# Performance work log

Hardware: AMD Instinct MI355X
Metric: run time of the kernel (lower is better)

Reference implementation:

```python
import jax, jax.numpy as jnp
import numpy as np

B, F, V, D_EMB = 16384, 32, 50000, 16
D_IN = F * D_EMB            # 512, concat embedding dim
N_TASK, N_SPEC, N_SH = 2, 2, 2
E = N_TASK * N_SPEC + N_SH  # 6 experts per CGC level
H1, H2 = 512, 256           # expert_params dims
T1, T2 = 128, 64            # tower dims


def setup_inputs() -> dict:
    key = jax.random.key(0)
    ks = iter(jax.random.split(key, 32))
    def w(shape, s=0.05):
        return jax.random.normal(next(ks), shape, jnp.float32) * s
    return dict(
        x_ids=jax.random.randint(next(ks), (B, F), 0, V),
        emb=w((F, V, D_EMB)),
        e1_W1=w((E, D_IN, H1)), e1_b1=jnp.zeros((E, H1), jnp.float32),
        e1_W2=w((E, H1, H2)), e1_b2=jnp.zeros((E, H2), jnp.float32),
        g1_Ws=w((N_TASK, D_IN, N_SPEC + N_SH)), g1_bs=jnp.zeros((N_TASK, N_SPEC + N_SH), jnp.float32),
        g1_Wsh=w((D_IN, E)), g1_bsh=jnp.zeros((E,), jnp.float32),
        e2_W1=w((E, H2, H1)), e2_b1=jnp.zeros((E, H1), jnp.float32),
        e2_W2=w((E, H1, H2)), e2_b2=jnp.zeros((E, H2), jnp.float32),
        g2_Ws=w((N_TASK, H2, N_SPEC + N_SH)), g2_bs=jnp.zeros((N_TASK, N_SPEC + N_SH), jnp.float32),
        tw_W1=w((N_TASK, H2, T1)), tw_b1=jnp.zeros((N_TASK, T1), jnp.float32),
        tw_W2=w((N_TASK, T1, T2)), tw_b2=jnp.zeros((N_TASK, T2), jnp.float32),
    )


def _cgc(x_list, W1, b1, W2, b2, Wg, bg, Wg_sh=None, bg_sh=None):
    # Stack expert inputs: task-t specific experts read x_list[t], shared read x_list[-1].
    X = jnp.stack([x_list[0]] * N_SPEC + [x_list[1]] * N_SPEC + [x_list[-1]] * N_SH)  # [E,B,Din]
    # Grouped two-layer expert MLP (BatchNorm is identity at eval-mode init).
    h = jax.nn.relu(jnp.einsum('ebd,edh->ebh', X, W1) + b1[:, None, :])   # [E,B,H1]
    out = jax.nn.relu(jnp.einsum('ebh,eho->ebo', h, W2) + b2[:, None, :])  # [E,B,H2]
    outs = []
    for t in range(N_TASK):
        gate = jax.nn.softmax(x_list[t] @ Wg[t] + bg[t], axis=-1)          # [B, N_SPEC+N_SH]
        sel = jnp.concatenate([out[t * N_SPEC:(t + 1) * N_SPEC], out[-N_SH:]], axis=0)
        outs.append(jnp.einsum('bk,kbo->bo', gate, sel))
    if Wg_sh is not None:  # shared gate only for levels < n_level
        gate = jax.nn.softmax(x_list[-1] @ Wg_sh + bg_sh, axis=-1)          # [B,E]
        outs.append(jnp.einsum('bk,kbo->bo', gate, out))
    return outs


def reference(x_ids, emb, e1_W1, e1_b1, e1_W2, e1_b2, g1_Ws, g1_bs, g1_Wsh, g1_bsh,
              e2_W1, e2_b1, e2_W2, e2_b2, g2_Ws, g2_bs, tw_W1, tw_b1, tw_W2, tw_b2):
    # Embedding lookup per sparse feature, then flatten (squeeze_dim=True).
    embed_x = emb[jnp.arange(F)[None, :], x_ids].reshape(B, D_IN)  # [B, 512]
    xs = [embed_x] * (N_TASK + 1)
    xs = _cgc(xs, e1_W1, e1_b1, e1_W2, e1_b2, g1_Ws, g1_bs, g1_Wsh, g1_bsh)  # level 1 -> 3 outs
    xs = _cgc(xs, e2_W1, e2_b1, e2_W2, e2_b2, g2_Ws, g2_bs)                  # level 2 -> 2 outs
    ys = []
    for t in range(N_TASK):
        h = jax.nn.relu(xs[t] @ tw_W1[t] + tw_b1[t])
        h = jax.nn.relu(h @ tw_W2[t] + tw_b2[t])
        ys.append(jax.nn.sigmoid(h))  # PredictionLayer('classification')
    return jnp.concatenate(ys, axis=1)  # [B, N_TASK*T2]
```

## Files before the change

### kernel.cpp

```cpp
#include <hip/hip_runtime.h>

typedef unsigned short u16;
typedef __attribute__((ext_vector_type(4))) unsigned short u16x4;
typedef __attribute__((ext_vector_type(8))) unsigned short u16x8;
typedef __attribute__((ext_vector_type(8))) short s16x8;
typedef __attribute__((ext_vector_type(4))) float f32x4;

#define BATCH 16384
#define NFEAT 32
#define NVOCAB 50000

__device__ __forceinline__ u16 f2bf(float f) {
    union { float f; unsigned u; } v; v.f = f;
    unsigned u = v.u;
    return (u16)((u + 0x7fffu + ((u >> 16) & 1u)) >> 16);
}
__device__ __forceinline__ float bf2f(u16 h) {
    union { unsigned u; float f; } v; v.u = ((unsigned)h) << 16;
    return v.f;
}

__device__ __forceinline__ void load_lds16(const u16* g, u16* l) {
    __builtin_amdgcn_global_load_lds(
        (const __attribute__((address_space(1))) void*)g,
        (__attribute__((address_space(3))) void*)l, 16, 0, 0);
}

struct PrepDesc { const float* src; u16* dst; int K; int N; int nz; int zbase; };
struct PrepArgs { PrepDesc d[6]; };

__global__ void prep_weights(PrepArgs args) {
    int z = blockIdx.z;
    int di = 0;
    #pragma unroll
    for (int i = 0; i < 6; i++)
        if (z >= args.d[i].zbase && z < args.d[i].zbase + args.d[i].nz) di = i;
    PrepDesc d = args.d[di];
    int zz = z - d.zbase;
    int k0 = blockIdx.x * 32, n0 = blockIdx.y * 32;
    if (k0 >= d.K || n0 >= d.N) return;
    __shared__ float tile[32][33];
    const float* src = d.src + (long)zz * d.K * d.N;
    u16* dst = d.dst + (long)zz * d.K * d.N;
    int tx = threadIdx.x & 31, ty = threadIdx.x >> 5;
    for (int r = ty; r < 32; r += 8) {
        int k = k0 + r, n = n0 + tx;
        tile[r][tx] = (k < d.K && n < d.N) ? src[(long)k * d.N + n] : 0.f;
    }
    __syncthreads();
    for (int r = ty; r < 32; r += 8) {
        int n = n0 + r, k = k0 + tx;
        if (n < d.N && k < d.K) dst[(long)n * d.K + k] = f2bf(tile[tx][r]);
    }
}

__global__ void gather_embed(const int* __restrict__ ids,
                             const float* __restrict__ emb,
                             u16* __restrict__ out) {
    int idx = blockIdx.x * 256 + threadIdx.x;
    int d4 = idx & 3;
    int f  = (idx >> 2) & 31;
    int b  = idx >> 7;
    int id = ids[b * NFEAT + f];
    const float4* p = (const float4*)(emb + ((long)f * NVOCAB + id) * 16) + d4;
    float4 v = *p;
    u16x4 o;
    o.x = f2bf(v.x); o.y = f2bf(v.y); o.z = f2bf(v.z); o.w = f2bf(v.w);
    *(u16x4*)(out + (long)b * 512 + f * 16 + d4 * 4) = o;
}

struct GemmP {
    const u16* A; const u16* Bt; const float* bias; u16* C;
    int N, K, a_zshift, c_row_stride; long a_zstride, c_zstride;
};

__device__ __forceinline__ void gemm_impl(const GemmP p) {
    __shared__ u16 sA[128 * 64];
    __shared__ u16 sB[256 * 64];
    const int z = blockIdx.z;
    const u16* Ab = p.A + (long)(z >> p.a_zshift) * p.a_zstride;
    const u16* Bb = p.Bt + (long)z * p.N * p.K;
    const int m0 = blockIdx.x * 128;
    const int n0 = blockIdx.y * 256;
    const int tid = threadIdx.x;
    const int lane = tid & 63;
    const int w = tid >> 6;
    const int wm = (w & 1) * 64;
    const int wn = (w >> 1) * 128;
    const int l16 = lane & 15;
    const int q = lane >> 4;
    const int key = l16 & 7;
    const int K = p.K;

    const int tr = tid >> 3;
    const int lc = (tid & 7) ^ (tr & 7);
    const u16* gA0 = Ab + (long)(m0 + tr) * K + lc * 8;
    const u16* gB0 = Bb + (long)(n0 + tr) * K + lc * 8;
    u16* lA0 = &sA[(tid & ~63) * 8];
    u16* lB0 = &sB[(tid & ~63) * 8];

    f32x4 acc[4][8] = {};

    for (int k0 = 0; k0 < K; k0 += 64) {
        if (k0) __syncthreads();
        #pragma unroll
        for (int i = 0; i < 4; i++)
            load_lds16(gA0 + (long)(32 * i) * K + k0, lA0 + i * 256 * 8);
        #pragma unroll
        for (int i = 0; i < 8; i++)
            load_lds16(gB0 + (long)(32 * i) * K + k0, lB0 + i * 256 * 8);
        __syncthreads();
        #pragma unroll
        for (int kk = 0; kk < 2; kk++) {
            const int pc = ((kk << 2) | q) ^ key;
            s16x8 af[4], bf[8];
            #pragma unroll
            for (int mt = 0; mt < 4; mt++)
                af[mt] = *(const s16x8*)(&sA[(wm + mt * 16 + l16) * 64 + pc * 8]);
            #pragma unroll
            for (int nt = 0; nt < 8; nt++)
                bf[nt] = *(const s16x8*)(&sB[(wn + nt * 16 + l16) * 64 + pc * 8]);
            #pragma unroll
            for (int mt = 0; mt < 4; mt++)
                #pragma unroll
                for (int nt = 0; nt < 8; nt++)
                    acc[mt][nt] = __builtin_amdgcn_mfma_f32_16x16x32_bf16(
                        bf[nt], af[mt], acc[mt][nt], 0, 0, 0);
        }
    }

    const float* bb = p.bias + (long)z * p.N;
    u16* Cp = p.C + (long)z * p.c_zstride;
    #pragma unroll
    for (int mt = 0; mt < 4; mt++) {
        int grow = m0 + wm + mt * 16 + l16;
        u16* rowp = Cp + (long)grow * p.c_row_stride;
        #pragma unroll
        for (int nt = 0; nt < 8; nt++) {
            int gc = n0 + wn + nt * 16 + q * 4;
            float4 bv = *(const float4*)(bb + gc);
            f32x4 v = acc[mt][nt];
            v.x = fmaxf(v.x + bv.x, 0.f);
            v.y = fmaxf(v.y + bv.y, 0.f);
            v.z = fmaxf(v.z + bv.z, 0.f);
            v.w = fmaxf(v.w + bv.w, 0.f);
            u16x4 o;
            o.x = f2bf(v.x); o.y = f2bf(v.y); o.z = f2bf(v.z); o.w = f2bf(v.w);
            *(u16x4*)(rowp + gc) = o;
        }
    }
}

__global__ __launch_bounds__(256, 2) void gemm_l1a(GemmP p) { gemm_impl(p); }
__global__ __launch_bounds__(256, 2) void gemm_l1b(GemmP p) { gemm_impl(p); }
__global__ __launch_bounds__(256, 2) void gemm_l2a(GemmP p) { gemm_impl(p); }
__global__ __launch_bounds__(256, 2) void gemm_l2b(GemmP p) { gemm_impl(p); }

__global__ __launch_bounds__(256, 1)
void tower_fused(const u16* __restrict__ x2, const u16* __restrict__ W1t,
                 const float* __restrict__ b1, const u16* __restrict__ W2t,
                 const float* __restrict__ b2, float* __restrict__ out) {
    const int t = blockIdx.y, m0 = blockIdx.x * 64;
    __shared__ u16 sX[64 * 256];
    __shared__ u16 sW1[128 * 256];
    __shared__ u16 sH[64 * 136];
    __shared__ u16 sW2[64 * 128];
    __shared__ float sB1[128];
    __shared__ float sB2[64];
    const int tid = threadIdx.x, lane = tid & 63, w = tid >> 6;
    const int l16 = lane & 15, q = lane >> 4;

    #pragma unroll
    for (int i = 0; i < 8; i++) {
        int c = i * 256 + tid, row = c >> 5, kc = c & 31;
        int lcc = (kc & ~7) | ((kc & 7) ^ (row & 7));
        load_lds16(x2 + ((long)t * BATCH + m0 + row) * 256 + lcc * 8,
                   &sX[(i * 256 + (tid & ~63)) * 8]);
    }
    #pragma unroll
    for (int i = 0; i < 16; i++) {
        int c = i * 256 + tid, row = c >> 5, kc = c & 31;
        int lcc = (kc & ~7) | ((kc & 7) ^ (row & 7));
        load_lds16(W1t + ((long)t * 128 + row) * 256 + lcc * 8,
                   &sW1[(i * 256 + (tid & ~63)) * 8]);
    }
    #pragma unroll
    for (int i = 0; i < 4; i++) {
        int c = i * 256 + tid, row = c >> 4, kc = c & 15;
        int lcc = (kc & ~7) | ((kc & 7) ^ (row & 7));
        load_lds16(W2t + ((long)t * 64 + row) * 128 + lcc * 8,
                   &sW2[(i * 256 + (tid & ~63)) * 8]);
    }
    if (tid < 128) sB1[tid] = b1[t * 128 + tid];
    if (tid < 64)  sB2[tid] = b2[t * 64 + tid];
    __syncthreads();

    f32x4 acc1[4][2] = {};
    #pragma unroll
    for (int kk = 0; kk < 8; kk++) {
        int pcb = kk * 4 + q;
        s16x8 af[4], bf[2];
        #pragma unroll
        for (int mt = 0; mt < 4; mt++) {
            int row = mt * 16 + l16;
            int sc = (pcb & ~7) | ((pcb & 7) ^ (row & 7));
            af[mt] = *(const s16x8*)(&sX[row * 256 + sc * 8]);
        }
        #pragma unroll
        for (int nt = 0; nt < 2; nt++) {
            int row = w * 32 + nt * 16 + l16;
            int sc = (pcb & ~7) | ((pcb & 7) ^ (row & 7));
            bf[nt] = *(const s16x8*)(&sW1[row * 256 + sc * 8]);
        }
        #pragma unroll
        for (int mt = 0; mt < 4; mt++)
            #pragma unroll
            for (int nt = 0; nt < 2; nt++)
                acc1[mt][nt] = __builtin_amdgcn_mfma_f32_16x16x32_bf16(
                    bf[nt], af[mt], acc1[mt][nt], 0, 0, 0);
    }
    #pragma unroll
    for (int mt = 0; mt < 4; mt++) {
        int row = mt * 16 + l16;
        #pragma unroll
        for (int nt = 0; nt < 2; nt++) {
            int col = w * 32 + nt * 16 + q * 4;
            f32x4 v = acc1[mt][nt];
            u16x4 o;
            o.x = f2bf(fmaxf(v.x + sB1[col + 0], 0.f));
            o.y = f2bf(fmaxf(v.y + sB1[col + 1], 0.f));
            o.z = f2bf(fmaxf(v.z + sB1[col + 2], 0.f));
            o.w = f2bf(fmaxf(v.w + sB1[col + 3], 0.f));
            *(u16x4*)(&sH[row * 136 + col]) = o;
        }
    }
    __syncthreads();

    f32x4 acc2[4] = {};
    #pragma unroll
    for (int kk = 0; kk < 4; kk++) {
        s16x8 af[4], bf;
        #pragma unroll
        for (int mt = 0; mt < 4; mt++) {
            int row = mt * 16 + l16;
            af[mt] = *(const s16x8*)(&sH[row * 136 + kk * 32 + q * 8]);
        }
        {
            int row = w * 16 + l16;
            int pc = kk * 4 + q;
            int sc = (pc & ~7) | ((pc & 7) ^ (row & 7));
            bf = *(const s16x8*)(&sW2[row * 128 + sc * 8]);
        }
        #pragma unroll
        for (int mt = 0; mt < 4; mt++)
            acc2[mt] = __builtin_amdgcn_mfma_f32_16x16x32_bf16(
                bf, af[mt], acc2[mt], 0, 0, 0);
    }
    #pragma unroll
    for (int mt = 0; mt < 4; mt++) {
        int grow = m0 + mt * 16 + l16;
        int col = w * 16 + q * 4;
        float4 bv = *(const float4*)(sB2 + col);
        f32x4 v = acc2[mt];
        float4 r;
        r.x = 1.f / (1.f + __expf(-(v.x + bv.x)));
        r.y = 1.f / (1.f + __expf(-(v.y + bv.y)));
        r.z = 1.f / (1.f + __expf(-(v.z + bv.z)));
        r.w = 1.f / (1.f + __expf(-(v.w + bv.w)));
        *(float4*)(out + (long)grow * 128 + t * 64 + col) = r;
    }
}

__global__ __launch_bounds__(256)
void gate1(const u16* __restrict__ embed, const u16* __restrict__ out1,
           const float* __restrict__ g1Ws, const float* __restrict__ g1bs,
           const float* __restrict__ gWsh, const float* __restrict__ gbsh,
           u16* __restrict__ x1) {
    const int m0 = blockIdx.x * 64;
    __shared__ float sg[64][16];
    const int tid = threadIdx.x;
    const int row = tid >> 2, pp = tid & 3;

    float a[4] = {0, 0, 0, 0}, b[4] = {0, 0, 0, 0}, c[6] = {0, 0, 0, 0, 0, 0};
    const u16* er = embed + (long)(m0 + row) * 512 + pp * 128;
    const float* Wa = g1Ws;
    const float* Wb = g1Ws + 2048;
    for (int j = 0; j < 128; j += 8) {
        u16x8 xv8 = *(const u16x8*)(er + j);
        #pragma unroll
        for (int u = 0; u < 8; u++) {
            float xv = bf2f(xv8[u]);
            int k = pp * 128 + j + u;
            float4 wa = *(const float4*)(Wa + k * 4);
            float4 wb = *(const float4*)(Wb + k * 4);
            a[0] += xv * wa.x; a[1] += xv * wa.y; a[2] += xv * wa.z; a[3] += xv * wa.w;
            b[0] += xv * wb.x; b[1] += xv * wb.y; b[2] += xv * wb.z; b[3] += xv * wb.w;
            const float* wc = gWsh + k * 6;
            #pragma unroll
            for (int g = 0; g < 6; g++) c[g] += xv * wc[g];
        }
    }
    #pragma unroll
    for (int g = 0; g < 4; g++) {
        a[g] += __shfl_xor(a[g], 1); a[g] += __shfl_xor(a[g], 2);
        b[g] += __shfl_xor(b[g], 1); b[g] += __shfl_xor(b[g], 2);
    }
    #pragma unroll
    for (int g = 0; g < 6; g++) { c[g] += __shfl_xor(c[g], 1); c[g] += __shfl_xor(c[g], 2); }
    if (pp == 0) {
        float mx, s, e[6];
        mx = -1e30f;
        for (int g = 0; g < 4; g++) { a[g] += g1bs[g]; mx = fmaxf(mx, a[g]); }
        s = 0.f; for (int g = 0; g < 4; g++) { e[g] = __expf(a[g] - mx); s += e[g]; }
        for (int g = 0; g < 4; g++) sg[row][g] = e[g] / s;
        mx = -1e30f;
        for (int g = 0; g < 4; g++) { b[g] += g1bs[4 + g]; mx = fmaxf(mx, b[g]); }
        s = 0.f; for (int g = 0; g < 4; g++) { e[g] = __expf(b[g] - mx); s += e[g]; }
        for (int g = 0; g < 4; g++) sg[row][4 + g] = e[g] / s;
        mx = -1e30f;
        for (int g = 0; g < 6; g++) { c[g] += gbsh[g]; mx = fmaxf(mx, c[g]); }
        s = 0.f; for (int g = 0; g < 6; g++) { e[g] = __expf(c[g] - mx); s += e[g]; }
        for (int g = 0; g < 6; g++) sg[row][8 + g] = e[g] / s;
    }
    __syncthreads();

    for (int r = 0; r < 64; r++) {
        long rb = m0 + r;
        float o[6];
        #pragma unroll
        for (int k = 0; k < 6; k++)
            o[k] = bf2f(out1[((long)k * BATCH + rb) * 256 + tid]);
        const float* g = sg[r];
        float v0 = g[0] * o[0] + g[1] * o[1] + g[2] * o[4] + g[3] * o[5];
        float v1 = g[4] * o[2] + g[5] * o[3] + g[6] * o[4] + g[7] * o[5];
        float v2 = 0.f;
        #pragma unroll
        for (int k = 0; k < 6; k++) v2 += g[8 + k] * o[k];
        x1[((long)0 * BATCH + rb) * 256 + tid] = f2bf(v0);
        x1[((long)1 * BATCH + rb) * 256 + tid] = f2bf(v1);
        x1[((long)2 * BATCH + rb) * 256 + tid] = f2bf(v2);
    }
}

__global__ __launch_bounds__(256)
void gate2(const u16* __restrict__ x1, const u16* __restrict__ out2,
           const float* __restrict__ g2Ws, const float* __restrict__ g2bs,
           u16* __restrict__ x2) {
    const int m0 = blockIdx.x * 64;
    __shared__ float sg[64][8];
    const int tid = threadIdx.x;
    const int row = tid >> 2, pp = tid & 3;

    float a[4] = {0, 0, 0, 0}, b[4] = {0, 0, 0, 0};
    const u16* e0 = x1 + ((long)0 * BATCH + m0 + row) * 256 + pp * 64;
    const u16* e1 = x1 + ((long)1 * BATCH + m0 + row) * 256 + pp * 64;
    const float* Wa = g2Ws;
    const float* Wb = g2Ws + 1024;
    for (int j = 0; j < 64; j += 8) {
        u16x8 x0 = *(const u16x8*)(e0 + j);
        u16x8 x1v = *(const u16x8*)(e1 + j);
        #pragma unroll
        for (int u = 0; u < 8; u++) {
            int k = pp * 64 + j + u;
            float4 wa = *(const float4*)(Wa + k * 4);
            float4 wb = *(const float4*)(Wb + k * 4);
            float xv0 = bf2f(x0[u]), xv1 = bf2f(x1v[u]);
            a[0] += xv0 * wa.x; a[1] += xv0 * wa.y; a[2] += xv0 * wa.z; a[3] += xv0 * wa.w;
            b[0] += xv1 * wb.x; b[1] += xv1 * wb.y; b[2] += xv1 * wb.z; b[3] += xv1 * wb.w;
        }
    }
    #pragma unroll
    for (int g = 0; g < 4; g++) {
        a[g] += __shfl_xor(a[g], 1); a[g] += __shfl_xor(a[g], 2);
        b[g] += __shfl_xor(b[g], 1); b[g] += __shfl_xor(b[g], 2);
    }
    if (pp == 0) {
        float mx, s, e[4];
        mx = -1e30f;
        for (int g = 0; g < 4; g++) { a[g] += g2bs[g]; mx = fmaxf(mx, a[g]); }
        s = 0.f; for (int g = 0; g < 4; g++) { e[g] = __expf(a[g] - mx); s += e[g]; }
        for (int g = 0; g < 4; g++) sg[row][g] = e[g] / s;
        mx = -1e30f;
        for (int g = 0; g < 4; g++) { b[g] += g2bs[4 + g]; mx = fmaxf(mx, b[g]); }
        s = 0.f; for (int g = 0; g < 4; g++) { e[g] = __expf(b[g] - mx); s += e[g]; }
        for (int g = 0; g < 4; g++) sg[row][4 + g] = e[g] / s;
    }
    __syncthreads();

    for (int r = 0; r < 64; r++) {
        long rb = m0 + r;
        float o[6];
        #pragma unroll
        for (int k = 0; k < 6; k++)
            o[k] = bf2f(out2[((long)k * BATCH + rb) * 256 + tid]);
        const float* g = sg[r];
        float v0 = g[0] * o[0] + g[1] * o[1] + g[2] * o[4] + g[3] * o[5];
        float v1 = g[4] * o[2] + g[5] * o[3] + g[6] * o[4] + g[7] * o[5];
        x2[((long)0 * BATCH + rb) * 256 + tid] = f2bf(v0);
        x2[((long)1 * BATCH + rb) * 256 + tid] = f2bf(v1);
    }
}

extern "C" void kernel_launch(void* const* d_in, const int* in_sizes, int n_in,
                              void* d_out, int out_size, void* d_ws, size_t ws_size,
                              hipStream_t stream) {
    const int*   x_ids = (const int*)  d_in[0];
    const float* emb   = (const float*)d_in[1];
    const float* e1W1  = (const float*)d_in[2];
    const float* e1b1  = (const float*)d_in[3];
    const float* e1W2  = (const float*)d_in[4];
    const float* e1b2  = (const float*)d_in[5];
    const float* g1Ws  = (const float*)d_in[6];
    const float* g1bs  = (const float*)d_in[7];
    const float* g1Wsh = (const float*)d_in[8];
    const float* g1bsh = (const float*)d_in[9];
    const float* e2W1  = (const float*)d_in[10];
    const float* e2b1  = (const float*)d_in[11];
    const float* e2W2  = (const float*)d_in[12];
    const float* e2b2  = (const float*)d_in[13];
    const float* g2Ws  = (const float*)d_in[14];
    const float* g2bs  = (const float*)d_in[15];
    const float* twW1  = (const float*)d_in[16];
    const float* twb1  = (const float*)d_in[17];
    const float* twW2  = (const float*)d_in[18];
    const float* twb2  = (const float*)d_in[19];
    float* out = (float*)d_out;

    char* ws = (char*)d_ws;
    u16* embed   = (u16*)(ws + 0);
    u16* wt_e1W1 = (u16*)(ws + 16777216);
    u16* wt_e1W2 = (u16*)(ws + 19922944);
    u16* wt_e2W1 = (u16*)(ws + 21495808);
    u16* wt_e2W2 = (u16*)(ws + 23068672);
    u16* wt_twW1 = (u16*)(ws + 24641536);
    u16* wt_twW2 = (u16*)(ws + 24772608);
    u16* h_buf   = (u16*)(ws + 24805376);
    u16* o_buf   = (u16*)(ws + 125468672);
    u16* x1      = (u16*)(ws + 175800320);
    u16* x2      = (u16*)(ws + 200966144);

    PrepArgs pa;
    pa.d[0] = { e1W1, wt_e1W1, 512, 512, 6,  0 };
    pa.d[1] = { e1W2, wt_e1W2, 512, 256, 6,  6 };
    pa.d[2] = { e2W1, wt_e2W1, 256, 512, 6, 12 };
    pa.d[3] = { e2W2, wt_e2W2, 512, 256, 6, 18 };
    pa.d[4] = { twW1, wt_twW1, 256, 128, 2, 24 };
    pa.d[5] = { twW2, wt_twW2, 128,  64, 2, 26 };
    prep_weights<<<dim3(16, 16, 28), 256, 0, stream>>>(pa);

    gather_embed<<<dim3(BATCH * NFEAT * 4 / 256), 256, 0, stream>>>(x_ids, emb, embed);

    GemmP p1a = { embed, wt_e1W1, e1b1, h_buf, 512, 512, 0, 512, 0L, (long)BATCH * 512 };
    gemm_l1a<<<dim3(128, 2, 6), 256, 0, stream>>>(p1a);

    GemmP p1b = { h_buf, wt_e1W2, e1b2, o_buf, 256, 512, 0, 256,
                  (long)BATCH * 512, (long)BATCH * 256 };
    gemm_l1b<<<dim3(128, 1, 6), 256, 0, stream>>>(p1b);

    gate1<<<dim3(BATCH / 64), 256, 0, stream>>>(embed, o_buf, g1Ws, g1bs, g1Wsh, g1bsh, x1);

    GemmP p2a = { x1, wt_e2W1, e2b1, h_buf, 512, 256, 1, 512,
                  (long)BATCH * 256, (long)BATCH * 512 };
    gemm_l2a<<<dim3(128, 2, 6), 256, 0, stream>>>(p2a);

    GemmP p2b = { h_buf, wt_e2W2, e2b2, o_buf, 256, 512, 0, 256,
                  (long)BATCH * 512, (long)BATCH * 256 };
    gemm_l2b<<<dim3(128, 1, 6), 256, 0, stream>>>(p2b);

    gate2<<<dim3(BATCH / 64), 256, 0, stream>>>(x1, o_buf, g2Ws, g2bs, x2);

    tower_fused<<<dim3(BATCH / 64, 2), 256, 0, stream>>>(x2, wt_twW1, twb1, wt_twW2, twb2, out);
}
```

Baseline: 547.4 us.

## Restructure gate kernels to 8 rows per block with vectorized combine

```diff
diff --git a/kernel.cpp b/kernel.cpp
--- a/kernel.cpp
+++ b/kernel.cpp
@@ -276,38 +276,41 @@
            const float* __restrict__ g1Ws, const float* __restrict__ g1bs,
            const float* __restrict__ gWsh, const float* __restrict__ gbsh,
            u16* __restrict__ x1) {
-    const int m0 = blockIdx.x * 64;
-    __shared__ float sg[64][16];
+    const int m0 = blockIdx.x * 8;
+    __shared__ float sg[8][16];
     const int tid = threadIdx.x;
-    const int row = tid >> 2, pp = tid & 3;
-
-    float a[4] = {0, 0, 0, 0}, b[4] = {0, 0, 0, 0}, c[6] = {0, 0, 0, 0, 0, 0};
-    const u16* er = embed + (long)(m0 + row) * 512 + pp * 128;
-    const float* Wa = g1Ws;
-    const float* Wb = g1Ws + 2048;
-    for (int j = 0; j < 128; j += 8) {
-        u16x8 xv8 = *(const u16x8*)(er + j);
-        #pragma unroll
-        for (int u = 0; u < 8; u++) {
-            float xv = bf2f(xv8[u]);
-            int k = pp * 128 + j + u;
-            float4 wa = *(const float4*)(Wa + k * 4);
-            float4 wb = *(const float4*)(Wb + k * 4);
+    const int row = tid >> 5, l = tid & 31;
+    const long rb = m0 + row;
+
+    float a[4] = {0,0,0,0}, b[4] = {0,0,0,0}, c[6] = {0,0,0,0,0,0};
+    {
+        const u16* er = embed + rb * 512 + l * 16;
+        u16x8 xa = *(const u16x8*)(er);
+        u16x8 xb = *(const u16x8*)(er + 8);
+        #pragma unroll
+        for (int u = 0; u < 16; u++) {
+            int k = l * 16 + u;
+            float xv = bf2f(u < 8 ? xa[u] : xb[u - 8]);
+            float4 wa = *(const float4*)(g1Ws + k * 4);
+            float4 wb = *(const float4*)(g1Ws + 2048 + k * 4);
             a[0] += xv * wa.x; a[1] += xv * wa.y; a[2] += xv * wa.z; a[3] += xv * wa.w;
             b[0] += xv * wb.x; b[1] += xv * wb.y; b[2] += xv * wb.z; b[3] += xv * wb.w;
-            const float* wc = gWsh + k * 6;
-            #pragma unroll
-            for (int g = 0; g < 6; g++) c[g] += xv * wc[g];
-        }
-    }
-    #pragma unroll
-    for (int g = 0; g < 4; g++) {
-        a[g] += __shfl_xor(a[g], 1); a[g] += __shfl_xor(a[g], 2);
-        b[g] += __shfl_xor(b[g], 1); b[g] += __shfl_xor(b[g], 2);
-    }
-    #pragma unroll
-    for (int g = 0; g < 6; g++) { c[g] += __shfl_xor(c[g], 1); c[g] += __shfl_xor(c[g], 2); }
-    if (pp == 0) {
+            float2 w0 = *(const float2*)(gWsh + k * 6);
+            float2 w1 = *(const float2*)(gWsh + k * 6 + 2);
+            float2 w2 = *(const float2*)(gWsh + k * 6 + 4);
+            c[0] += xv * w0.x; c[1] += xv * w0.y;
+            c[2] += xv * w1.x; c[3] += xv * w1.y;
+            c[4] += xv * w2.x; c[5] += xv * w2.y;
+        }
+    }
+    #pragma unroll
+    for (int off = 1; off < 32; off <<= 1) {
+        #pragma unroll
+        for (int g = 0; g < 4; g++) { a[g] += __shfl_xor(a[g], off); b[g] += __shfl_xor(b[g], off); }
+        #pragma unroll
+        for (int g = 0; g < 6; g++) c[g] += __shfl_xor(c[g], off);
+    }
+    if (l == 0) {
         float mx, s, e[6];
         mx = -1e30f;
         for (int g = 0; g < 4; g++) { a[g] += g1bs[g]; mx = fmaxf(mx, a[g]); }
@@ -324,57 +327,58 @@
     }
     __syncthreads();
 
-    for (int r = 0; r < 64; r++) {
-        long rb = m0 + r;
-        float o[6];
-        #pragma unroll
-        for (int k = 0; k < 6; k++)
-            o[k] = bf2f(out1[((long)k * BATCH + rb) * 256 + tid]);
-        const float* g = sg[r];
-        float v0 = g[0] * o[0] + g[1] * o[1] + g[2] * o[4] + g[3] * o[5];
-        float v1 = g[4] * o[2] + g[5] * o[3] + g[6] * o[4] + g[7] * o[5];
-        float v2 = 0.f;
-        #pragma unroll
-        for (int k = 0; k < 6; k++) v2 += g[8 + k] * o[k];
-        x1[((long)0 * BATCH + rb) * 256 + tid] = f2bf(v0);
-        x1[((long)1 * BATCH + rb) * 256 + tid] = f2bf(v1);
-        x1[((long)2 * BATCH + rb) * 256 + tid] = f2bf(v2);
-    }
+    const int c8 = l * 8;
+    const u16* ob = out1 + rb * 256 + c8;
+    u16x8 o[6];
+    #pragma unroll
+    for (int k = 0; k < 6; k++) o[k] = *(const u16x8*)(ob + (long)k * BATCH * 256);
+    const float* g = sg[row];
+    u16x8 r0, r1, r2;
+    #pragma unroll
+    for (int u = 0; u < 8; u++) {
+        float o0 = bf2f(o[0][u]), o1 = bf2f(o[1][u]), o2 = bf2f(o[2][u]);
+        float o3 = bf2f(o[3][u]), o4 = bf2f(o[4][u]), o5 = bf2f(o[5][u]);
+        r0[u] = f2bf(g[0] * o0 + g[1] * o1 + g[2] * o4 + g[3] * o5);
+        r1[u] = f2bf(g[4] * o2 + g[5] * o3 + g[6] * o4 + g[7] * o5);
+        r2[u] = f2bf(g[8] * o0 + g[9] * o1 + g[10] * o2 + g[11] * o3 + g[12] * o4 + g[13] * o5);
+    }
+    *(u16x8*)(x1 + ((long)0 * BATCH + rb) * 256 + c8) = r0;
+    *(u16x8*)(x1 + ((long)1 * BATCH + rb) * 256 + c8) = r1;
+    *(u16x8*)(x1 + ((long)2 * BATCH + rb) * 256 + c8) = r2;
 }
 
 __global__ __launch_bounds__(256)
 void gate2(const u16* __restrict__ x1, const u16* __restrict__ out2,
            const float* __restrict__ g2Ws, const float* __restrict__ g2bs,
            u16* __restrict__ x2) {
-    const int m0 = blockIdx.x * 64;
-    __shared__ float sg[64][8];
+    const int m0 = blockIdx.x * 8;
+    __shared__ float sg[8][8];
     const int tid = threadIdx.x;
-    const int row = tid >> 2, pp = tid & 3;
-
-    float a[4] = {0, 0, 0, 0}, b[4] = {0, 0, 0, 0};
-    const u16* e0 = x1 + ((long)0 * BATCH + m0 + row) * 256 + pp * 64;
-    const u16* e1 = x1 + ((long)1 * BATCH + m0 + row) * 256 + pp * 64;
-    const float* Wa = g2Ws;
-    const float* Wb = g2Ws + 1024;
-    for (int j = 0; j < 64; j += 8) {
-        u16x8 x0 = *(const u16x8*)(e0 + j);
-        u16x8 x1v = *(const u16x8*)(e1 + j);
+    const int row = tid >> 5, l = tid & 31;
+    const long rb = m0 + row;
+
+    float a[4] = {0,0,0,0}, b[4] = {0,0,0,0};
+    {
+        const u16* e0 = x1 + rb * 256 + l * 8;
+        const u16* e1 = e0 + (long)BATCH * 256;
+        u16x8 x0 = *(const u16x8*)e0;
+        u16x8 x1v = *(const u16x8*)e1;
         #pragma unroll
         for (int u = 0; u < 8; u++) {
-            int k = pp * 64 + j + u;
-            float4 wa = *(const float4*)(Wa + k * 4);
-            float4 wb = *(const float4*)(Wb + k * 4);
+            int k = l * 8 + u;
+            float4 wa = *(const float4*)(g2Ws + k * 4);
+            float4 wb = *(const float4*)(g2Ws + 1024 + k * 4);
             float xv0 = bf2f(x0[u]), xv1 = bf2f(x1v[u]);
             a[0] += xv0 * wa.x; a[1] += xv0 * wa.y; a[2] += xv0 * wa.z; a[3] += xv0 * wa.w;
             b[0] += xv1 * wb.x; b[1] += xv1 * wb.y; b[2] += xv1 * wb.z; b[3] += xv1 * wb.w;
         }
     }
     #pragma unroll
-    for (int g = 0; g < 4; g++) {
-        a[g] += __shfl_xor(a[g], 1); a[g] += __shfl_xor(a[g], 2);
-        b[g] += __shfl_xor(b[g], 1); b[g] += __shfl_xor(b[g], 2);
-    }
-    if (pp == 0) {
+    for (int off = 1; off < 32; off <<= 1) {
+        #pragma unroll
+        for (int g = 0; g < 4; g++) { a[g] += __shfl_xor(a[g], off); b[g] += __shfl_xor(b[g], off); }
+    }
+    if (l == 0) {
         float mx, s, e[4];
         mx = -1e30f;
         for (int g = 0; g < 4; g++) { a[g] += g2bs[g]; mx = fmaxf(mx, a[g]); }
@@ -387,18 +391,22 @@
     }
     __syncthreads();
 
-    for (int r = 0; r < 64; r++) {
-        long rb = m0 + r;
-        float o[6];
-        #pragma unroll
-        for (int k = 0; k < 6; k++)
-            o[k] = bf2f(out2[((long)k * BATCH + rb) * 256 + tid]);
-        const float* g = sg[r];
-        float v0 = g[0] * o[0] + g[1] * o[1] + g[2] * o[4] + g[3] * o[5];
-        float v1 = g[4] * o[2] + g[5] * o[3] + g[6] * o[4] + g[7] * o[5];
-        x2[((long)0 * BATCH + rb) * 256 + tid] = f2bf(v0);
-        x2[((long)1 * BATCH + rb) * 256 + tid] = f2bf(v1);
-    }
+    const int c8 = l * 8;
+    const u16* ob = out2 + rb * 256 + c8;
+    u16x8 o[6];
+    #pragma unroll
+    for (int k = 0; k < 6; k++) o[k] = *(const u16x8*)(ob + (long)k * BATCH * 256);
+    const float* g = sg[row];
+    u16x8 r0, r1;
+    #pragma unroll
+    for (int u = 0; u < 8; u++) {
+        float o0 = bf2f(o[0][u]), o1 = bf2f(o[1][u]), o2 = bf2f(o[2][u]);
+        float o3 = bf2f(o[3][u]), o4 = bf2f(o[4][u]), o5 = bf2f(o[5][u]);
+        r0[u] = f2bf(g[0] * o0 + g[1] * o1 + g[2] * o4 + g[3] * o5);
+        r1[u] = f2bf(g[4] * o2 + g[5] * o3 + g[6] * o4 + g[7] * o5);
+    }
+    *(u16x8*)(x2 + ((long)0 * BATCH + rb) * 256 + c8) = r0;
+    *(u16x8*)(x2 + ((long)1 * BATCH + rb) * 256 + c8) = r1;
 }
 
 extern "C" void kernel_launch(void* const* d_in, const int* in_sizes, int n_in,
@@ -457,7 +465,7 @@
                   (long)BATCH * 512, (long)BATCH * 256 };
     gemm_l1b<<<dim3(128, 1, 6), 256, 0, stream>>>(p1b);
 
-    gate1<<<dim3(BATCH / 64), 256, 0, stream>>>(embed, o_buf, g1Ws, g1bs, g1Wsh, g1bsh, x1);
+    gate1<<<dim3(BATCH / 8), 256, 0, stream>>>(embed, o_buf, g1Ws, g1bs, g1Wsh, g1bsh, x1);
 
     GemmP p2a = { x1, wt_e2W1, e2b1, h_buf, 512, 256, 1, 512,
                   (long)BATCH * 256, (long)BATCH * 512 };
@@ -467,7 +475,7 @@
                   (long)BATCH * 512, (long)BATCH * 256 };
     gemm_l2b<<<dim3(128, 1, 6), 256, 0, stream>>>(p2b);
 
-    gate2<<<dim3(BATCH / 64), 256, 0, stream>>>(x1, o_buf, g2Ws, g2bs, x2);
+    gate2<<<dim3(BATCH / 8), 256, 0, stream>>>(x1, o_buf, g2Ws, g2bs, x2);
 
     tower_fused<<<dim3(BATCH / 64, 2), 256, 0, stream>>>(x2, wt_twW1, twb1, wt_twW2, twb2, out);
 }
```

After: 522.7 us. 4.5% less time.
